# Kernel optimization log

Hardware: AMD Instinct MI355X
Metric: run time of the kernel (lower is better)

The kernel has to match this reference:

```python
import jax, jax.numpy as jnp
import numpy as np

N_FILTERS = 8
FILTER_LEN = 31
PAD = (FILTER_LEN - 1) // 2  # 15
B, L = 64, 131072


def setup_inputs() -> dict:
    key = jax.random.key(0)
    ks = jax.random.split(key, 7)
    x = jax.random.normal(ks[0], (B, L), dtype=jnp.float32)
    features = jax.random.normal(ks[1], (B, N_FILTERS), dtype=jnp.float32)
    # learned params
    filter_params = jax.random.normal(ks[2], (N_FILTERS, 1, FILTER_LEN), dtype=jnp.float32)
    # selector MLP (torch Linear convention: W is (out, in))
    lim = 1.0 / np.sqrt(N_FILTERS)
    W1 = jax.random.uniform(ks[3], (N_FILTERS, N_FILTERS), minval=-lim, maxval=lim, dtype=jnp.float32)
    b1 = jax.random.uniform(ks[4], (N_FILTERS,), minval=-lim, maxval=lim, dtype=jnp.float32)
    W2 = jax.random.uniform(ks[5], (N_FILTERS, N_FILTERS), minval=-lim, maxval=lim, dtype=jnp.float32)
    b2 = jax.random.uniform(ks[6], (N_FILTERS,), minval=-lim, maxval=lim, dtype=jnp.float32)
    return {"x": x, "features": features, "filter_params": filter_params,
            "W1": W1, "b1": b1, "W2": W2, "b2": b2}


def reference(x, features, filter_params, W1, b1, W2, b2):
    # conv1d (cross-correlation, as in torch): (B,1,L) * (F,1,K) -> (B,F,L)
    xp = x[:, None, :]
    filtered = jax.lax.conv_general_dilated(
        xp, filter_params,
        window_strides=(1,), padding=[(PAD, PAD)],
        dimension_numbers=('NCH', 'OIH', 'NCH'))
    # per-sample soft filter selection
    h = jax.nn.relu(features @ W1.T + b1)
    weights = jax.nn.softmax(h @ W2.T + b2, axis=-1)  # (B, F)
    # weighted sum over filter channels -> (B, L)
    out = jnp.einsum('bfl,bf->bl', filtered, weights)
    return out
```

## Files before the change

### kernel.cpp

```cpp
#include <hip/hip_runtime.h>
#include <math.h>

#define BB 64
#define LL 131072
#define NF 8
#define FLEN 31

#define TPB 256
#define RPT 8
#define TILE (TPB * RPT)
#define TCELLS (TILE / 4)
#define NCELLS (TCELLS + 8)
#define ROWCELLS (LL / 4)

typedef float f32x4 __attribute__((ext_vector_type(4)));

#define SWZ(c) ((c) ^ (((c) >> 3) & 7))

__global__ __launch_bounds__(TPB, 6) void adaptive_filter_fused(
    const float* __restrict__ x,
    const float* __restrict__ features,
    const float* __restrict__ fp,
    const float* __restrict__ W1,
    const float* __restrict__ b1,
    const float* __restrict__ W2,
    const float* __restrict__ b2,
    float* __restrict__ out)
{
    const int tiles_per_row = LL / TILE;
    const int row  = blockIdx.x / tiles_per_row;
    const int tile = blockIdx.x % tiles_per_row;
    const int tid  = threadIdx.x;

    __shared__ f32x4 lds4[NCELLS];
    __shared__ float cs[32];

    const f32x4* xrow4 = reinterpret_cast<const f32x4*>(x + (size_t)row * LL);
    const int cell_base = tile * TCELLS - 4;

    const int d0 = tid, d1 = tid + TPB, d2 = tid + 2 * TPB;
    const unsigned gc0 = (unsigned)(cell_base + d0);
    const unsigned gc1 = (unsigned)(cell_base + d1);
    const unsigned gc2 = (unsigned)(cell_base + d2);
    f32x4 v0 = (f32x4)(0.0f);
    f32x4 v1 = v0, v2 = v0;
    if (gc0 < ROWCELLS) v0 = __builtin_nontemporal_load(&xrow4[gc0]);
    if (gc1 < ROWCELLS) v1 = __builtin_nontemporal_load(&xrow4[gc1]);
    const bool has2 = (tid < NCELLS - 2 * TPB);
    if (has2 && gc2 < ROWCELLS) v2 = __builtin_nontemporal_load(&xrow4[gc2]);

    if (tid < FLEN) {
        const int t = tid;
        float f[NF];
        #pragma unroll
        for (int j = 0; j < NF; ++j) f[j] = features[row * NF + j];

        float h[NF];
        #pragma unroll
        for (int i = 0; i < NF; ++i) {
            float s = b1[i];
            #pragma unroll
            for (int j = 0; j < NF; ++j) s = fmaf(f[j], W1[i * NF + j], s);
            h[i] = fmaxf(s, 0.0f);
        }

        float w[NF];
        float m = -1e30f;
        #pragma unroll
        for (int i = 0; i < NF; ++i) {
            float s = b2[i];
            #pragma unroll
            for (int j = 0; j < NF; ++j) s = fmaf(h[j], W2[i * NF + j], s);
            w[i] = s;
            m = fmaxf(m, s);
        }
        float denom = 0.0f;
        #pragma unroll
        for (int i = 0; i < NF; ++i) { w[i] = expf(w[i] - m); denom += w[i]; }
        const float inv = 1.0f / denom;

        float s = 0.0f;
        #pragma unroll
        for (int ff = 0; ff < NF; ++ff) s = fmaf(w[ff] * inv, fp[ff * FLEN + t], s);
        cs[t] = s;
    }

    lds4[SWZ(d0)] = v0;
    lds4[SWZ(d1)] = v1;
    if (has2) lds4[SWZ(d2)] = v2;

    __syncthreads();

    const float tv = cs[tid & 31];
    float tap[FLEN];
    #pragma unroll
    for (int t = 0; t < FLEN; ++t)
        tap[t] = __int_as_float(__builtin_amdgcn_readlane(__float_as_int(tv), t));

    float wA[20], wB[20];
    #pragma unroll
    for (int k = 0; k < 5; ++k) {
        const f32x4 v = lds4[SWZ(2 * tid + k)];
        wA[4 * k + 0] = v.x; wA[4 * k + 1] = v.y;
        wA[4 * k + 2] = v.z; wA[4 * k + 3] = v.w;
    }
    #pragma unroll
    for (int k = 0; k < 5; ++k) {
        const f32x4 v = lds4[SWZ(2 * tid + 5 + k)];
        wB[4 * k + 0] = v.x; wB[4 * k + 1] = v.y;
        wB[4 * k + 2] = v.z; wB[4 * k + 3] = v.w;
    }

    float acc[RPT];
    #pragma unroll
    for (int r = 0; r < RPT; ++r) acc[r] = 0.0f;

    #pragma unroll
    for (int r = 0; r < RPT; ++r) {
        #pragma unroll
        for (int t = 0; t <= 18 - r; ++t)
            acc[r] = fmaf(tap[t], wA[r + 1 + t], acc[r]);
        #pragma unroll
        for (int t = 19 - r; t < FLEN; ++t)
            acc[r] = fmaf(tap[t], wB[r + t - 19], acc[r]);
    }

    f32x4* orow4 = reinterpret_cast<f32x4*>(out + (size_t)row * LL) + tile * TCELLS;
    f32x4 s0; s0.x = acc[0]; s0.y = acc[1]; s0.z = acc[2]; s0.w = acc[3];
    f32x4 s1; s1.x = acc[4]; s1.y = acc[5]; s1.z = acc[6]; s1.w = acc[7];
    __builtin_nontemporal_store(s0, &orow4[2 * tid + 0]);
    __builtin_nontemporal_store(s1, &orow4[2 * tid + 1]);
}

extern "C" void kernel_launch(void* const* d_in, const int* in_sizes, int n_in,
                              void* d_out, int out_size, void* d_ws, size_t ws_size,
                              hipStream_t stream) {
    const float* x        = (const float*)d_in[0];
    const float* features = (const float*)d_in[1];
    const float* fp       = (const float*)d_in[2];
    const float* W1       = (const float*)d_in[3];
    const float* b1       = (const float*)d_in[4];
    const float* W2       = (const float*)d_in[5];
    const float* b2       = (const float*)d_in[6];
    float* out = (float*)d_out;

    const int grid = BB * (LL / TILE);
    adaptive_filter_fused<<<grid, TPB, 0, stream>>>(x, features, fp, W1, b1, W2, b2, out);
}
```

Measured before the change: 19.04 us.

## Give each wave its own LDS halo tile and drop block barrier

Splits the block tile into per-wave sub-tiles, each with its own halo region and its own copy of the combined filter taps, so every wave loads, stages and consumes only its own data. This lets the block-wide __syncthreads be removed and avoids waves waiting on each other. In exchange it loads extra halo cells per wave, has every wave recompute the selector MLP, and uses more LDS. There is no wave-level barrier or fence between the LDS writes and reads, relying on in-order execution within a wave.

Measured after the change: 22.02 us. +15.6%, slower.

```diff
diff --git a/kernel.cpp b/kernel.cpp
--- a/kernel.cpp
+++ b/kernel.cpp
@@ -7,10 +7,12 @@
 #define FLEN 31
 
 #define TPB 256
+#define NWAVE 4
 #define RPT 8
 #define TILE (TPB * RPT)
 #define TCELLS (TILE / 4)
-#define NCELLS (TCELLS + 8)
+#define WCELLS 128
+#define WSTAGE (WCELLS + 8)
 #define ROWCELLS (LL / 4)
 
 typedef float f32x4 __attribute__((ext_vector_type(4)));
@@ -31,26 +33,29 @@
     const int row  = blockIdx.x / tiles_per_row;
     const int tile = blockIdx.x % tiles_per_row;
     const int tid  = threadIdx.x;
+    const int wv   = tid >> 6;
+    const int ln   = tid & 63;
 
-    __shared__ f32x4 lds4[NCELLS];
-    __shared__ float cs[32];
+    __shared__ f32x4 lds4[NWAVE][WSTAGE];
+    __shared__ float cs[NWAVE][32];
 
     const f32x4* xrow4 = reinterpret_cast<const f32x4*>(x + (size_t)row * LL);
-    const int cell_base = tile * TCELLS - 4;
+    const int wcell0 = tile * TCELLS + wv * WCELLS;
+    const int cell_base = wcell0 - 4;
 
-    const int d0 = tid, d1 = tid + TPB, d2 = tid + 2 * TPB;
+    const int d0 = ln, d1 = ln + 64;
     const unsigned gc0 = (unsigned)(cell_base + d0);
     const unsigned gc1 = (unsigned)(cell_base + d1);
-    const unsigned gc2 = (unsigned)(cell_base + d2);
     f32x4 v0 = (f32x4)(0.0f);
     f32x4 v1 = v0, v2 = v0;
     if (gc0 < ROWCELLS) v0 = __builtin_nontemporal_load(&xrow4[gc0]);
     if (gc1 < ROWCELLS) v1 = __builtin_nontemporal_load(&xrow4[gc1]);
-    const bool has2 = (tid < NCELLS - 2 * TPB);
+    const bool has2 = (ln < WSTAGE - 128);
+    const unsigned gc2 = (unsigned)(cell_base + ln + 128);
     if (has2 && gc2 < ROWCELLS) v2 = __builtin_nontemporal_load(&xrow4[gc2]);
 
-    if (tid < FLEN) {
-        const int t = tid;
+    if (ln < FLEN) {
+        const int t = ln;
         float f[NF];
         #pragma unroll
         for (int j = 0; j < NF; ++j) f[j] = features[row * NF + j];
@@ -82,16 +87,15 @@
         float s = 0.0f;
         #pragma unroll
         for (int ff = 0; ff < NF; ++ff) s = fmaf(w[ff] * inv, fp[ff * FLEN + t], s);
-        cs[t] = s;
+        cs[wv][t] = s;
     }
 
-    lds4[SWZ(d0)] = v0;
-    lds4[SWZ(d1)] = v1;
-    if (has2) lds4[SWZ(d2)] = v2;
+    lds4[wv][SWZ(d0)] = v0;
+    lds4[wv][SWZ(d1)] = v1;
+    if (has2) lds4[wv][SWZ(ln + 128)] = v2;
 
-    __syncthreads();
 
-    const float tv = cs[tid & 31];
+    const float tv = cs[wv][ln & 31];
     float tap[FLEN];
     #pragma unroll
     for (int t = 0; t < FLEN; ++t)
@@ -100,13 +104,13 @@
     float wA[20], wB[20];
     #pragma unroll
     for (int k = 0; k < 5; ++k) {
-        const f32x4 v = lds4[SWZ(2 * tid + k)];
+        const f32x4 v = lds4[wv][SWZ(2 * ln + k)];
         wA[4 * k + 0] = v.x; wA[4 * k + 1] = v.y;
         wA[4 * k + 2] = v.z; wA[4 * k + 3] = v.w;
     }
     #pragma unroll
     for (int k = 0; k < 5; ++k) {
-        const f32x4 v = lds4[SWZ(2 * tid + 5 + k)];
+        const f32x4 v = lds4[wv][SWZ(2 * ln + 5 + k)];
         wB[4 * k + 0] = v.x; wB[4 * k + 1] = v.y;
         wB[4 * k + 2] = v.z; wB[4 * k + 3] = v.w;
     }
@@ -125,11 +129,11 @@
             acc[r] = fmaf(tap[t], wB[r + t - 19], acc[r]);
     }
 
-    f32x4* orow4 = reinterpret_cast<f32x4*>(out + (size_t)row * LL) + tile * TCELLS;
+    f32x4* orow4 = reinterpret_cast<f32x4*>(out + (size_t)row * LL) + wcell0;
     f32x4 s0; s0.x = acc[0]; s0.y = acc[1]; s0.z = acc[2]; s0.w = acc[3];
     f32x4 s1; s1.x = acc[4]; s1.y = acc[5]; s1.z = acc[6]; s1.w = acc[7];
-    __builtin_nontemporal_store(s0, &orow4[2 * tid + 0]);
-    __builtin_nontemporal_store(s1, &orow4[2 * tid + 1]);
+    __builtin_nontemporal_store(s0, &orow4[2 * ln + 0]);
+    __builtin_nontemporal_store(s1, &orow4[2 * ln + 1]);
 }
 
 extern "C" void kernel_launch(void* const* d_in, const int* in_sizes, int n_in,
```
